# Performance work log

Hardware: AMD Instinct MI355X
Metric: run time of the kernel (lower is better)

The kernel has to match this reference:

```python
import jax, jax.numpy as jnp
import numpy as np

B, C, L, N = 2, 8, 128, 48  # volume side L, kept size N per axis (fact=4 -> N >= L/4)


def setup_inputs() -> dict:
    key = jax.random.key(0)
    ks = jax.random.split(key, 7)
    x = jax.random.normal(ks[0], (B, C, L, L, L), dtype=jnp.float32)
    EN3 = jax.random.normal(ks[1], (L, N), dtype=jnp.float32)
    EN2 = jax.random.normal(ks[2], (L, N), dtype=jnp.float32)
    EN1 = jax.random.normal(ks[3], (L, N), dtype=jnp.float32)
    DE3 = jax.random.normal(ks[4], (N, L), dtype=jnp.float32)
    DE2 = jax.random.normal(ks[5], (N, L), dtype=jnp.float32)
    DE1 = jax.random.normal(ks[6], (N, L), dtype=jnp.float32)
    return {"x": x, "EN3": EN3, "EN2": EN2, "EN1": EN1,
            "DE3": DE3, "DE2": DE2, "DE1": DE1}


def reference(x, EN3, EN2, EN1, DE3, DE2, DE1):
    # ---- encode: contract D (axis -3) with EN3, H (axis -2) with EN2, W (axis -1) with EN1
    e = jnp.einsum('bcdhw,dp->bcphw', x, EN3)
    e = jnp.einsum('bcphw,hq->bcpqw', e, EN2)
    enc = jnp.einsum('bcpqw,wr->bcpqr', e, EN1)  # (B,C,N,N,N)
    # ---- decode: three application orders of DE1/DE2/DE3, averaged (as in source)
    # order W,H,D
    y = jnp.einsum('bcpqr,rw->bcpqw', enc, DE1)
    y = jnp.einsum('bcpqw,qh->bcphw', y, DE2)
    y1 = jnp.einsum('bcphw,pd->bcdhw', y, DE3)
    # order H,D,W
    y = jnp.einsum('bcpqr,qh->bcphr', enc, DE2)
    y = jnp.einsum('bcphr,pd->bcdhr', y, DE3)
    y2 = jnp.einsum('bcdhr,rw->bcdhw', y, DE1)
    # order D,W,H
    y = jnp.einsum('bcpqr,pd->bcdqr', enc, DE3)
    y = jnp.einsum('bcdqr,rw->bcdqw', y, DE1)
    y3 = jnp.einsum('bcdqw,qh->bcdhw', y, DE2)
    return (y1 + y2 + y3) / 3.0
```

## Files before the change

kernel.cpp:

```cpp
#include <hip/hip_runtime.h>


#define LDIM 128
#define NDIM 48
#define HW   (LDIM * LDIM)
#define L3V  (LDIM * HW)

typedef __bf16 bf16x8 __attribute__((ext_vector_type(8)));
typedef float  f32x4  __attribute__((ext_vector_type(4)));
typedef unsigned short u16;

#define S128 136
#define S64  72

#define W_EN3T 0
#define W_EN2T 6144
#define W_EN1T 12288
#define W_DE3T 18432
#define W_DE2T 26624
#define W_DE1T 34816
#define W_TOT  43008

__device__ __forceinline__ u16 f2bf(float f) {
    unsigned int u = __builtin_bit_cast(unsigned int, f);
    return (u16)((u + 0x7fffu + ((u >> 16) & 1u)) >> 16);
}
__device__ __forceinline__ bf16x8 frag(const u16* p) {
    return *reinterpret_cast<const bf16x8*>(p);
}
__device__ __forceinline__ f32x4 mfma16(bf16x8 a, bf16x8 b, f32x4 c) {
    return __builtin_amdgcn_mfma_f32_16x16x32_bf16(a, b, c, 0, 0, 0);
}

__global__ __launch_bounds__(256) void kPrep(const float* __restrict__ EN3,
                                             const float* __restrict__ EN2,
                                             const float* __restrict__ EN1,
                                             const float* __restrict__ DE3,
                                             const float* __restrict__ DE2,
                                             const float* __restrict__ DE1,
                                             u16* __restrict__ W) {
    int i = blockIdx.x * 256 + threadIdx.x;
    if (i < 6144)       { int p = i >> 7, d = i & 127;                 W[i] = f2bf(EN3[d * 48 + p]); }
    else if (i < 12288) { int j = i - 6144;  int q = j >> 7, h = j & 127; W[i] = f2bf(EN2[h * 48 + q]); }
    else if (i < 18432) { int j = i - 12288; int r = j >> 7, w = j & 127; W[i] = f2bf(EN1[w * 48 + r]); }
    else if (i < 26624) { int j = i - 18432; int d = j >> 6, p = j & 63;  W[i] = f2bf(p < 48 ? DE3[p * 128 + d] : 0.f); }
    else if (i < 34816) { int j = i - 26624; int h = j >> 6, q = j & 63;  W[i] = f2bf(q < 48 ? DE2[q * 128 + h] : 0.f); }
    else if (i < 43008) { int j = i - 34816; int w = j >> 6, r = j & 63;  W[i] = f2bf(r < 48 ? DE1[r * 128 + w] : 0.f); }
}

__global__ __launch_bounds__(256) void kA(const float* __restrict__ x,
                                          const u16* __restrict__ W,
                                          u16* __restrict__ t1) {
    __shared__ u16 lx[128 * S128];
    const int bc = blockIdx.y;
    const int d  = blockIdx.x;
    const int t = threadIdx.x, lane = t & 63, wv = t >> 6, quad = lane >> 4;
    const int row = lane & 15, kof = quad * 8;

    {
        const float* xp = x + (size_t)bc * L3V + (size_t)d * HW;
        for (int i = 0; i < 16; ++i) {
            int f = i * 1024 + t * 4;
            float4 v = *reinterpret_cast<const float4*>(xp + f);
            int h = f >> 7, w = f & 127;
            uint2 pk;
            pk.x = (unsigned)f2bf(v.x) | ((unsigned)f2bf(v.y) << 16);
            pk.y = (unsigned)f2bf(v.z) | ((unsigned)f2bf(v.w) << 16);
            *reinterpret_cast<uint2*>(lx + h * S128 + w) = pk;
        }
    }
    __syncthreads();
    const int h0 = wv * 32;
    f32x4 acc[2][3] = {};
    for (int kk = 0; kk < 4; ++kk) {
        bf16x8 b[3];
        for (int n = 0; n < 3; ++n)
            b[n] = frag(W + W_EN1T + (n * 16 + row) * 128 + kk * 32 + kof);
        for (int m = 0; m < 2; ++m) {
            bf16x8 a = frag(lx + (h0 + m * 16 + row) * S128 + kk * 32 + kof);
            for (int n = 0; n < 3; ++n) acc[m][n] = mfma16(a, b[n], acc[m][n]);
        }
    }
    u16* op = t1 + (size_t)bc * 48 * HW + d * 128;
    for (int m = 0; m < 2; ++m)
        for (int n = 0; n < 3; ++n) {
            int r = n * 16 + row;
            int h = h0 + m * 16 + quad * 4;
            uint2 pk;
            pk.x = (unsigned)f2bf(acc[m][n][0]) | ((unsigned)f2bf(acc[m][n][1]) << 16);
            pk.y = (unsigned)f2bf(acc[m][n][2]) | ((unsigned)f2bf(acc[m][n][3]) << 16);
            *reinterpret_cast<uint2*>(op + (size_t)r * HW + h) = pk;
        }
}

__global__ __launch_bounds__(256) void kMid(const u16* __restrict__ t1,
                                            const u16* __restrict__ W,
                                            u16* __restrict__ u2) {
    __shared__ u16 pool[26624];
    u16* lT = pool;
    u16* lE = pool + 6528;
    u16* lO = pool;
    u16* lU = pool + 17408;

    const int slab = blockIdx.x;
    const int t = threadIdx.x, lane = t & 63, wv = t >> 6, quad = lane >> 4;
    const int row = lane & 15, kof = quad * 8;
    const u16* Sg = t1 + (size_t)slab * HW;

    for (int i = t; i < 48 * 16; i += 256)  { int p = i >> 4; lE[p * S64 + 48 + (i & 15)] = 0; }
    for (int i = t; i < 128 * 16; i += 256) { int h = i >> 4; lU[h * S64 + 48 + (i & 15)] = 0; }

    {
        const int d0 = wv * 32;
        f32x4 acc[2][3] = {};
        for (int kk = 0; kk < 4; ++kk) {
            bf16x8 b[3];
            for (int n = 0; n < 3; ++n)
                b[n] = frag(W + W_EN2T + (n * 16 + row) * 128 + kk * 32 + kof);
            for (int m = 0; m < 2; ++m) {
                bf16x8 a = frag(Sg + (d0 + m * 16 + row) * 128 + kk * 32 + kof);
                for (int n = 0; n < 3; ++n) acc[m][n] = mfma16(a, b[n], acc[m][n]);
            }
        }
        for (int m = 0; m < 2; ++m)
            for (int n = 0; n < 3; ++n) {
                int q = n * 16 + row;
                int dd = d0 + m * 16 + quad * 4;
                uint2 pk;
                pk.x = (unsigned)f2bf(acc[m][n][0]) | ((unsigned)f2bf(acc[m][n][1]) << 16);
                pk.y = (unsigned)f2bf(acc[m][n][2]) | ((unsigned)f2bf(acc[m][n][3]) << 16);
                *reinterpret_cast<uint2*>(lT + q * S128 + dd) = pk;
            }
    }
    __syncthreads();
    if (wv < 3) {
        const int p0 = wv * 16;
        f32x4 acc[3] = {};
        for (int kk = 0; kk < 4; ++kk) {
            bf16x8 a = frag(W + W_EN3T + (p0 + row) * 128 + kk * 32 + kof);
            for (int n = 0; n < 3; ++n) {
                bf16x8 b = frag(lT + (n * 16 + row) * S128 + kk * 32 + kof);
                acc[n] = mfma16(a, b, acc[n]);
            }
        }
        for (int n = 0; n < 3; ++n)
            for (int j = 0; j < 4; ++j)
                lE[(p0 + quad * 4 + j) * S64 + n * 16 + row] = f2bf(acc[n][j]);
    }
    __syncthreads();
    {
        const int h0 = wv * 32;
        f32x4 acc[2][3] = {};
        for (int kk = 0; kk < 2; ++kk) {
            bf16x8 b[3];
            for (int n = 0; n < 3; ++n)
                b[n] = frag(lE + (n * 16 + row) * S64 + kk * 32 + kof);
            for (int m = 0; m < 2; ++m) {
                bf16x8 a = frag(W + W_DE2T + (h0 + m * 16 + row) * 64 + kk * 32 + kof);
                for (int n = 0; n < 3; ++n) acc[m][n] = mfma16(a, b[n], acc[m][n]);
            }
        }
        for (int m = 0; m < 2; ++m)
            for (int n = 0; n < 3; ++n)
                for (int j = 0; j < 4; ++j)
                    lU[(h0 + m * 16 + quad * 4 + j) * S64 + n * 16 + row] = f2bf(acc[m][n][j]);
    }
    __syncthreads();
    {
        const int m0 = (wv & 1) * 64, n0 = (wv >> 1) * 64;
        f32x4 acc[4][4] = {};
        for (int kk = 0; kk < 2; ++kk) {
            bf16x8 b[4];
            for (int n = 0; n < 4; ++n)
                b[n] = frag(lU + (n0 + n * 16 + row) * S64 + kk * 32 + kof);
            for (int m = 0; m < 4; ++m) {
                bf16x8 a = frag(W + W_DE3T + (m0 + m * 16 + row) * 64 + kk * 32 + kof);
                for (int n = 0; n < 4; ++n) acc[m][n] = mfma16(a, b[n], acc[m][n]);
            }
        }
        for (int m = 0; m < 4; ++m)
            for (int n = 0; n < 4; ++n)
                for (int j = 0; j < 4; ++j)
                    lO[(m0 + m * 16 + quad * 4 + j) * S128 + n0 + n * 16 + row] = f2bf(acc[m][n][j]);
    }
    __syncthreads();
    u16* up = u2 + (size_t)slab * HW;
    for (int i = 0; i < 8; ++i) {
        int idx = t + i * 256;
        int h = idx >> 4, c = (idx & 15) * 8;
        *reinterpret_cast<float4*>(up + h * 128 + c) =
            *reinterpret_cast<const float4*>(lO + h * S128 + c);
    }
}

__global__ __launch_bounds__(256) void kF(const u16* __restrict__ u2,
                                          const u16* __restrict__ W,
                                          float* __restrict__ out) {
    __shared__ u16 lb[128 * S64];
    const int bc = blockIdx.y, dh0 = blockIdx.x * 128;
    const int t = threadIdx.x, lane = t & 63, wv = t >> 6, quad = lane >> 4;
    const int row = lane & 15, kof = quad * 8;
    const int m0 = (wv & 1) * 64, n0 = (wv >> 1) * 64;

    bf16x8 bfr[4][2];
    for (int n = 0; n < 4; ++n)
        for (int kk = 0; kk < 2; ++kk)
            bfr[n][kk] = frag(W + W_DE1T + (n0 + n * 16 + row) * 64 + kk * 32 + kof);

    {
        const int r   = t & 63;
        const int dhb = (t >> 6) * 32;
        const u16* sp = u2 + ((size_t)(bc * 48) + r) * HW + dh0 + dhb;
        const bool valid = r < 48;
        for (int i = 0; i < 4; ++i) {
            u16 v[8] = {0, 0, 0, 0, 0, 0, 0, 0};
            if (valid) *reinterpret_cast<float4*>(v) = *reinterpret_cast<const float4*>(sp + i * 8);
            for (int j = 0; j < 8; ++j) lb[(dhb + i * 8 + j) * S64 + r] = v[j];
        }
    }
    __syncthreads();
    f32x4 acc[4][4] = {};
    for (int kk = 0; kk < 2; ++kk) {
        bf16x8 a[4];
        for (int m = 0; m < 4; ++m)
            a[m] = frag(lb + (m0 + m * 16 + row) * S64 + kk * 32 + kof);
        for (int m = 0; m < 4; ++m)
            for (int n = 0; n < 4; ++n) acc[m][n] = mfma16(a[m], bfr[n][kk], acc[m][n]);
    }
    float* ob = out + (size_t)bc * L3V + (size_t)dh0 * 128;
    for (int m = 0; m < 4; ++m)
        for (int n = 0; n < 4; ++n)
            for (int j = 0; j < 4; ++j) {
                int dh = m0 + m * 16 + quad * 4 + j;
                int wp = n0 + n * 16 + row;
                ob[(size_t)dh * 128 + wp] = acc[m][n][j];
            }
}

extern "C" void kernel_launch(void* const* d_in, const int* in_sizes, int n_in,
                              void* d_out, int out_size, void* d_ws, size_t ws_size,
                              hipStream_t stream) {
    const float* x   = (const float*)d_in[0];
    const float* EN3 = (const float*)d_in[1];
    const float* EN2 = (const float*)d_in[2];
    const float* EN1 = (const float*)d_in[3];
    const float* DE3 = (const float*)d_in[4];
    const float* DE2 = (const float*)d_in[5];
    const float* DE1 = (const float*)d_in[6];
    float* out = (float*)d_out;

    u16* t1 = (u16*)d_ws;
    u16* u2 = (u16*)((char*)d_ws + 25165824);
    u16* W  = (u16*)((char*)d_ws + 50331648);

    kPrep<<<dim3(168),     256, 0, stream>>>(EN3, EN2, EN1, DE3, DE2, DE1, W);
    kA   <<<dim3(128, 16), 256, 0, stream>>>(x, W, t1);
    kMid <<<dim3(768),     256, 0, stream>>>(t1, W, u2);
    kF   <<<dim3(128, 16), 256, 0, stream>>>(u2, W, out);
}
```

Before: 283.4 us.

## Precompute EN3·DE3 product and restructure pipeline around D-axis slab GEMM

New measurement: 279.6 us. No clear change (-1.3%).

```diff
diff --git a/kernel.cpp b/kernel.cpp
--- a/kernel.cpp
+++ b/kernel.cpp
@@ -5,6 +5,7 @@
 #define NDIM 48
 #define HW   (LDIM * LDIM)
 #define L3V  (LDIM * HW)
+#define QR   2304
 
 typedef __bf16 bf16x8 __attribute__((ext_vector_type(8)));
 typedef float  f32x4  __attribute__((ext_vector_type(4)));
@@ -19,7 +20,8 @@
 #define W_DE3T 18432
 #define W_DE2T 26624
 #define W_DE1T 34816
-#define W_TOT  43008
+#define W_M    43008
+#define W_TOT  59392
 
 __device__ __forceinline__ u16 f2bf(float f) {
     unsigned int u = __builtin_bit_cast(unsigned int, f);
@@ -46,106 +48,133 @@
     else if (i < 26624) { int j = i - 18432; int d = j >> 6, p = j & 63;  W[i] = f2bf(p < 48 ? DE3[p * 128 + d] : 0.f); }
     else if (i < 34816) { int j = i - 26624; int h = j >> 6, q = j & 63;  W[i] = f2bf(q < 48 ? DE2[q * 128 + h] : 0.f); }
     else if (i < 43008) { int j = i - 34816; int w = j >> 6, r = j & 63;  W[i] = f2bf(r < 48 ? DE1[r * 128 + w] : 0.f); }
-}
-
-__global__ __launch_bounds__(256) void kA(const float* __restrict__ x,
-                                          const u16* __restrict__ W,
-                                          u16* __restrict__ t1) {
-    __shared__ u16 lx[128 * S128];
-    const int bc = blockIdx.y;
-    const int d  = blockIdx.x;
-    const int t = threadIdx.x, lane = t & 63, wv = t >> 6, quad = lane >> 4;
+    else if (i < 59392) {
+        int j = i - 43008; int dp = j >> 7, d = j & 127;
+        float s = 0.f;
+        for (int p = 0; p < 48; ++p) s += EN3[d * 48 + p] * DE3[p * 128 + dp];
+        W[i] = f2bf(s);
+    }
+}
+
+__global__ __launch_bounds__(256) void kEnc(const float* __restrict__ x,
+                                            const u16* __restrict__ W,
+                                            u16* __restrict__ t) {
+    __shared__ u16 lS[128 * S128];
+    __shared__ u16 lT[48 * S128];
+    const int bc = blockIdx.y, d = blockIdx.x;
+    const int tid = threadIdx.x, lane = tid & 63, wv = tid >> 6, quad = lane >> 4;
     const int row = lane & 15, kof = quad * 8;
 
     {
         const float* xp = x + (size_t)bc * L3V + (size_t)d * HW;
         for (int i = 0; i < 16; ++i) {
-            int f = i * 1024 + t * 4;
+            int f = i * 1024 + tid * 4;
             float4 v = *reinterpret_cast<const float4*>(xp + f);
             int h = f >> 7, w = f & 127;
             uint2 pk;
             pk.x = (unsigned)f2bf(v.x) | ((unsigned)f2bf(v.y) << 16);
             pk.y = (unsigned)f2bf(v.z) | ((unsigned)f2bf(v.w) << 16);
-            *reinterpret_cast<uint2*>(lx + h * S128 + w) = pk;
-        }
-    }
-    __syncthreads();
-    const int h0 = wv * 32;
-    f32x4 acc[2][3] = {};
-    for (int kk = 0; kk < 4; ++kk) {
-        bf16x8 b[3];
-        for (int n = 0; n < 3; ++n)
-            b[n] = frag(W + W_EN1T + (n * 16 + row) * 128 + kk * 32 + kof);
-        for (int m = 0; m < 2; ++m) {
-            bf16x8 a = frag(lx + (h0 + m * 16 + row) * S128 + kk * 32 + kof);
-            for (int n = 0; n < 3; ++n) acc[m][n] = mfma16(a, b[n], acc[m][n]);
-        }
-    }
-    u16* op = t1 + (size_t)bc * 48 * HW + d * 128;
-    for (int m = 0; m < 2; ++m)
-        for (int n = 0; n < 3; ++n) {
-            int r = n * 16 + row;
-            int h = h0 + m * 16 + quad * 4;
-            uint2 pk;
-            pk.x = (unsigned)f2bf(acc[m][n][0]) | ((unsigned)f2bf(acc[m][n][1]) << 16);
-            pk.y = (unsigned)f2bf(acc[m][n][2]) | ((unsigned)f2bf(acc[m][n][3]) << 16);
-            *reinterpret_cast<uint2*>(op + (size_t)r * HW + h) = pk;
-        }
-}
-
-__global__ __launch_bounds__(256) void kMid(const u16* __restrict__ t1,
-                                            const u16* __restrict__ W,
-                                            u16* __restrict__ u2) {
-    __shared__ u16 pool[26624];
-    u16* lT = pool;
-    u16* lE = pool + 6528;
-    u16* lO = pool;
-    u16* lU = pool + 17408;
-
-    const int slab = blockIdx.x;
-    const int t = threadIdx.x, lane = t & 63, wv = t >> 6, quad = lane >> 4;
-    const int row = lane & 15, kof = quad * 8;
-    const u16* Sg = t1 + (size_t)slab * HW;
-
-    for (int i = t; i < 48 * 16; i += 256)  { int p = i >> 4; lE[p * S64 + 48 + (i & 15)] = 0; }
-    for (int i = t; i < 128 * 16; i += 256) { int h = i >> 4; lU[h * S64 + 48 + (i & 15)] = 0; }
-
-    {
-        const int d0 = wv * 32;
+            *reinterpret_cast<uint2*>(lS + h * S128 + w) = pk;
+        }
+    }
+    __syncthreads();
+    {
+        const int h0 = wv * 32;
         f32x4 acc[2][3] = {};
         for (int kk = 0; kk < 4; ++kk) {
             bf16x8 b[3];
             for (int n = 0; n < 3; ++n)
-                b[n] = frag(W + W_EN2T + (n * 16 + row) * 128 + kk * 32 + kof);
+                b[n] = frag(W + W_EN1T + (n * 16 + row) * 128 + kk * 32 + kof);
             for (int m = 0; m < 2; ++m) {
-                bf16x8 a = frag(Sg + (d0 + m * 16 + row) * 128 + kk * 32 + kof);
+                bf16x8 a = frag(lS + (h0 + m * 16 + row) * S128 + kk * 32 + kof);
                 for (int n = 0; n < 3; ++n) acc[m][n] = mfma16(a, b[n], acc[m][n]);
             }
         }
         for (int m = 0; m < 2; ++m)
             for (int n = 0; n < 3; ++n) {
-                int q = n * 16 + row;
-                int dd = d0 + m * 16 + quad * 4;
+                int r = n * 16 + row, h = h0 + m * 16 + quad * 4;
                 uint2 pk;
                 pk.x = (unsigned)f2bf(acc[m][n][0]) | ((unsigned)f2bf(acc[m][n][1]) << 16);
                 pk.y = (unsigned)f2bf(acc[m][n][2]) | ((unsigned)f2bf(acc[m][n][3]) << 16);
-                *reinterpret_cast<uint2*>(lT + q * S128 + dd) = pk;
+                *reinterpret_cast<uint2*>(lT + r * S128 + h) = pk;
             }
     }
     __syncthreads();
     if (wv < 3) {
-        const int p0 = wv * 16;
+        const int q0 = wv * 16;
         f32x4 acc[3] = {};
         for (int kk = 0; kk < 4; ++kk) {
-            bf16x8 a = frag(W + W_EN3T + (p0 + row) * 128 + kk * 32 + kof);
+            bf16x8 a = frag(W + W_EN2T + (q0 + row) * 128 + kk * 32 + kof);
             for (int n = 0; n < 3; ++n) {
                 bf16x8 b = frag(lT + (n * 16 + row) * S128 + kk * 32 + kof);
                 acc[n] = mfma16(a, b, acc[n]);
             }
         }
+        u16* tp = t + (size_t)(bc * 128 + d) * QR;
         for (int n = 0; n < 3; ++n)
             for (int j = 0; j < 4; ++j)
-                lE[(p0 + quad * 4 + j) * S64 + n * 16 + row] = f2bf(acc[n][j]);
+                tp[(q0 + quad * 4 + j) * 48 + n * 16 + row] = f2bf(acc[n][j]);
+    }
+}
+
+__global__ __launch_bounds__(256) void kM(const u16* __restrict__ t,
+                                          const u16* __restrict__ W,
+                                          u16* __restrict__ u) {
+    __shared__ u16 lB[64 * S128];
+    const int bc = blockIdx.y, qr0 = blockIdx.x * 64;
+    const int tid = threadIdx.x, lane = tid & 63, wv = tid >> 6, quad = lane >> 4;
+    const int row = lane & 15, kof = quad * 8;
+
+    {
+        const u16* tp = t + (size_t)bc * (128 * QR) + qr0 + (tid & 7) * 8;
+        const int d0 = tid >> 3;
+        for (int g = 0; g < 4; ++g) {
+            int dd = d0 + g * 32;
+            u16 v[8];
+            *reinterpret_cast<float4*>(v) = *reinterpret_cast<const float4*>(tp + (size_t)dd * QR);
+            for (int j = 0; j < 8; ++j) lB[((tid & 7) * 8 + j) * S128 + dd] = v[j];
+        }
+    }
+    __syncthreads();
+    const int m0 = wv * 32;
+    f32x4 acc[2][4] = {};
+    for (int kk = 0; kk < 4; ++kk) {
+        bf16x8 a[2], b[4];
+        for (int n = 0; n < 4; ++n)
+            b[n] = frag(lB + (n * 16 + row) * S128 + kk * 32 + kof);
+        for (int m = 0; m < 2; ++m)
+            a[m] = frag(W + W_M + (m0 + m * 16 + row) * 128 + kk * 32 + kof);
+        for (int m = 0; m < 2; ++m)
+            for (int n = 0; n < 4; ++n) acc[m][n] = mfma16(a[m], b[n], acc[m][n]);
+    }
+    u16* up = u + (size_t)bc * (128 * QR) + qr0;
+    for (int m = 0; m < 2; ++m)
+        for (int n = 0; n < 4; ++n)
+            for (int j = 0; j < 4; ++j) {
+                int dp = m0 + m * 16 + quad * 4 + j;
+                up[(size_t)dp * QR + n * 16 + row] = f2bf(acc[m][n][j]);
+            }
+}
+
+__global__ __launch_bounds__(256) void kDec(const u16* __restrict__ u,
+                                            const u16* __restrict__ W,
+                                            float* __restrict__ out) {
+    __shared__ u16 lU[48 * S64];
+    __shared__ u16 lV[128 * S64];
+    const int bc = blockIdx.y, dp = blockIdx.x;
+    const int tid = threadIdx.x, lane = tid & 63, wv = tid >> 6, quad = lane >> 4;
+    const int row = lane & 15, kof = quad * 8;
+
+    for (int i = tid; i < 48 * 16; i += 256)  lU[(i >> 4) * S64 + 48 + (i & 15)] = 0;
+    for (int i = tid; i < 128 * 16; i += 256) lV[(i >> 4) * S64 + 48 + (i & 15)] = 0;
+    {
+        const u16* sp = u + (size_t)(bc * 128 + dp) * QR;
+        for (int i = tid; i < 288; i += 256) {
+            u16 v[8];
+            *reinterpret_cast<float4*>(v) = *reinterpret_cast<const float4*>(sp + i * 8);
+            int q = i / 6, rb = (i % 6) * 8;
+            for (int j = 0; j < 8; ++j) lU[(rb + j) * S64 + q] = v[j];
+        }
     }
     __syncthreads();
     {
@@ -154,7 +183,7 @@
         for (int kk = 0; kk < 2; ++kk) {
             bf16x8 b[3];
             for (int n = 0; n < 3; ++n)
-                b[n] = frag(lE + (n * 16 + row) * S64 + kk * 32 + kof);
+                b[n] = frag(lU + (n * 16 + row) * S64 + kk * 32 + kof);
             for (int m = 0; m < 2; ++m) {
                 bf16x8 a = frag(W + W_DE2T + (h0 + m * 16 + row) * 64 + kk * 32 + kof);
                 for (int n = 0; n < 3; ++n) acc[m][n] = mfma16(a, b[n], acc[m][n]);
@@ -163,78 +192,27 @@
         for (int m = 0; m < 2; ++m)
             for (int n = 0; n < 3; ++n)
                 for (int j = 0; j < 4; ++j)
-                    lU[(h0 + m * 16 + quad * 4 + j) * S64 + n * 16 + row] = f2bf(acc[m][n][j]);
-    }
-    __syncthreads();
-    {
-        const int m0 = (wv & 1) * 64, n0 = (wv >> 1) * 64;
-        f32x4 acc[4][4] = {};
+                    lV[(h0 + m * 16 + quad * 4 + j) * S64 + n * 16 + row] = f2bf(acc[m][n][j]);
+    }
+    __syncthreads();
+    {
+        const int h0 = wv * 32;
+        f32x4 acc[2][8] = {};
         for (int kk = 0; kk < 2; ++kk) {
-            bf16x8 b[4];
-            for (int n = 0; n < 4; ++n)
-                b[n] = frag(lU + (n0 + n * 16 + row) * S64 + kk * 32 + kof);
-            for (int m = 0; m < 4; ++m) {
-                bf16x8 a = frag(W + W_DE3T + (m0 + m * 16 + row) * 64 + kk * 32 + kof);
-                for (int n = 0; n < 4; ++n) acc[m][n] = mfma16(a, b[n], acc[m][n]);
-            }
-        }
-        for (int m = 0; m < 4; ++m)
-            for (int n = 0; n < 4; ++n)
+            bf16x8 a[2], b[8];
+            for (int n = 0; n < 8; ++n)
+                b[n] = frag(W + W_DE1T + (n * 16 + row) * 64 + kk * 32 + kof);
+            for (int m = 0; m < 2; ++m)
+                a[m] = frag(lV + (h0 + m * 16 + row) * S64 + kk * 32 + kof);
+            for (int m = 0; m < 2; ++m)
+                for (int n = 0; n < 8; ++n) acc[m][n] = mfma16(a[m], b[n], acc[m][n]);
+        }
+        float* ob = out + (size_t)bc * L3V + (size_t)dp * HW;
+        for (int m = 0; m < 2; ++m)
+            for (int n = 0; n < 8; ++n)
                 for (int j = 0; j < 4; ++j)
-                    lO[(m0 + m * 16 + quad * 4 + j) * S128 + n0 + n * 16 + row] = f2bf(acc[m][n][j]);
-    }
-    __syncthreads();
-    u16* up = u2 + (size_t)slab * HW;
-    for (int i = 0; i < 8; ++i) {
-        int idx = t + i * 256;
-        int h = idx >> 4, c = (idx & 15) * 8;
-        *reinterpret_cast<float4*>(up + h * 128 + c) =
-            *reinterpret_cast<const float4*>(lO + h * S128 + c);
-    }
-}
-
-__global__ __launch_bounds__(256) void kF(const u16* __restrict__ u2,
-                                          const u16* __restrict__ W,
-                                          float* __restrict__ out) {
-    __shared__ u16 lb[128 * S64];
-    const int bc = blockIdx.y, dh0 = blockIdx.x * 128;
-    const int t = threadIdx.x, lane = t & 63, wv = t >> 6, quad = lane >> 4;
-    const int row = lane & 15, kof = quad * 8;
-    const int m0 = (wv & 1) * 64, n0 = (wv >> 1) * 64;
-
-    bf16x8 bfr[4][2];
-    for (int n = 0; n < 4; ++n)
-        for (int kk = 0; kk < 2; ++kk)
-            bfr[n][kk] = frag(W + W_DE1T + (n0 + n * 16 + row) * 64 + kk * 32 + kof);
-
-    {
-        const int r   = t & 63;
-        const int dhb = (t >> 6) * 32;
-        const u16* sp = u2 + ((size_t)(bc * 48) + r) * HW + dh0 + dhb;
-        const bool valid = r < 48;
-        for (int i = 0; i < 4; ++i) {
-            u16 v[8] = {0, 0, 0, 0, 0, 0, 0, 0};
-            if (valid) *reinterpret_cast<float4*>(v) = *reinterpret_cast<const float4*>(sp + i * 8);
-            for (int j = 0; j < 8; ++j) lb[(dhb + i * 8 + j) * S64 + r] = v[j];
-        }
-    }
-    __syncthreads();
-    f32x4 acc[4][4] = {};
-    for (int kk = 0; kk < 2; ++kk) {
-        bf16x8 a[4];
-        for (int m = 0; m < 4; ++m)
-            a[m] = frag(lb + (m0 + m * 16 + row) * S64 + kk * 32 + kof);
-        for (int m = 0; m < 4; ++m)
-            for (int n = 0; n < 4; ++n) acc[m][n] = mfma16(a[m], bfr[n][kk], acc[m][n]);
-    }
-    float* ob = out + (size_t)bc * L3V + (size_t)dh0 * 128;
-    for (int m = 0; m < 4; ++m)
-        for (int n = 0; n < 4; ++n)
-            for (int j = 0; j < 4; ++j) {
-                int dh = m0 + m * 16 + quad * 4 + j;
-                int wp = n0 + n * 16 + row;
-                ob[(size_t)dh * 128 + wp] = acc[m][n][j];
-            }
+                    ob[(h0 + m * 16 + quad * 4 + j) * 128 + n * 16 + row] = acc[m][n][j];
+    }
 }
 
 extern "C" void kernel_launch(void* const* d_in, const int* in_sizes, int n_in,
@@ -249,12 +227,12 @@
     const float* DE1 = (const float*)d_in[6];
     float* out = (float*)d_out;
 
-    u16* t1 = (u16*)d_ws;
-    u16* u2 = (u16*)((char*)d_ws + 25165824);
-    u16* W  = (u16*)((char*)d_ws + 50331648);
-
-    kPrep<<<dim3(168),     256, 0, stream>>>(EN3, EN2, EN1, DE3, DE2, DE1, W);
-    kA   <<<dim3(128, 16), 256, 0, stream>>>(x, W, t1);
-    kMid <<<dim3(768),     256, 0, stream>>>(t1, W, u2);
-    kF   <<<dim3(128, 16), 256, 0, stream>>>(u2, W, out);
-}
+    u16* t = (u16*)d_ws;
+    u16* u = (u16*)((char*)d_ws + 9437184);
+    u16* W = (u16*)((char*)d_ws + 18874368);
+
+    kPrep<<<dim3(232),     256, 0, stream>>>(EN3, EN2, EN1, DE3, DE2, DE1, W);
+    kEnc <<<dim3(128, 16), 256, 0, stream>>>(x, W, t);
+    kM   <<<dim3(36, 16),  256, 0, stream>>>(t, W, u);
+    kDec <<<dim3(128, 16), 256, 0, stream>>>(u, W, out);
+}
```
